# Kernel optimization log

Hardware: AMD Instinct MI355X
Metric: run time of the kernel (lower is better)

Reference implementation:

```python
import jax, jax.numpy as jnp
import numpy as np

N = 50000      # nodes in batched graph
E = 1600000    # edges (avg degree ~32)
D = 64         # feature width (features_dim = h_dim = out_dim)
R = 4          # num_rels (bond types)
L = 4          # RGCN layers: i2h + 2 hidden + h2o
B = 256        # graphs in the batch
NEG_SLOPE = 0.2


def setup_inputs() -> dict:
    key = jax.random.key(0)
    ks = jax.random.split(key, 12)
    h = jax.random.normal(ks[0], (N, D), jnp.float32)
    src = jax.random.randint(ks[1], (E,), 0, N, jnp.int32)
    dst = jax.random.randint(ks[2], (E,), 0, N, jnp.int32)
    etypes = jax.random.randint(ks[3], (E,), 0, R, jnp.int32)
    gids = jnp.sort(jax.random.randint(ks[4], (N,), 0, B, jnp.int32))
    Wrel = jax.random.normal(ks[5], (L, R, D, D), jnp.float32) * 0.05
    Wloop = jax.random.normal(ks[6], (L, D, D), jnp.float32) * 0.05
    brel = jnp.zeros((L, D), jnp.float32)
    Wg = jax.random.normal(ks[7], (D, D), jnp.float32) * 0.05
    al = jax.random.normal(ks[8], (D,), jnp.float32) * 0.05
    ar = jax.random.normal(ks[9], (D,), jnp.float32) * 0.05
    Wd = jax.random.normal(ks[10], (D, 1), jnp.float32) * 0.05
    bd = jnp.zeros((1,), jnp.float32)
    return dict(h=h, Wrel=Wrel, Wloop=Wloop, brel=brel, Wg=Wg, al=al, ar=ar,
                Wd=Wd, bd=bd, src=src, dst=dst, etypes=etypes, gids=gids)


def reference(h, Wrel, Wloop, brel, Wg, al, ar, Wd, bd, src, dst, etypes, gids):
    n = h.shape[0]
    # --- stacked RelGraphConv layers (basis regularizer with num_bases=num_rels
    # -> per-relation weight), self-loop + bias + ReLU, sum aggregation ---
    for l in range(Wrel.shape[0]):
        hr = jnp.einsum('nd,rdo->nro', h, Wrel[l])          # [N, R, D]
        msg = hr[src, etypes]                                # [E, D] gather
        agg = jax.ops.segment_sum(msg, dst, num_segments=n)  # [N, D] scatter-add
        h = jax.nn.relu(agg + h @ Wloop[l] + brel[l])
    # --- GATConv, 1 head ---
    z = h @ Wg                                               # [N, D]
    el = z @ al                                              # [N] a_l . z
    er = z @ ar                                              # [N] a_r . z
    e = jax.nn.leaky_relu(el[src] + er[dst], NEG_SLOPE)      # [E]
    m = jax.ops.segment_max(e, dst, num_segments=n)          # edge-softmax (stable)
    ex = jnp.exp(e - m[dst])
    den = jax.ops.segment_sum(ex, dst, num_segments=n)
    alpha = ex / jnp.maximum(den[dst], 1e-9)                 # [E]
    hg = jax.ops.segment_sum(alpha[:, None] * z[src], dst, num_segments=n)  # [N, D]
    # --- SumPooling over each graph, view [N,1,D] -> pooled [B,1,D] ---
    pooled = jax.ops.segment_sum(hg, gids, num_segments=B)[:, None, :]
    # --- dense head ---
    return pooled @ Wd + bd                                  # [B, 1, 1]
```

## Files before the change

### kernel.cpp

```cpp
#include <hip/hip_runtime.h>

#define DD 64
#define EPB 1024
#define NREP 8

typedef float f32x4 __attribute__((ext_vector_type(4)));
typedef float f32x8 __attribute__((ext_vector_type(8)));
typedef __bf16 bf16x8 __attribute__((ext_vector_type(8)));

__device__ __forceinline__ unsigned enc_f32(float x) {
  unsigned u = __float_as_uint(x);
  return (u & 0x80000000u) ? ~u : (u | 0x80000000u);
}
__device__ __forceinline__ float dec_f32(unsigned k) {
  return (k & 0x80000000u) ? __uint_as_float(k ^ 0x80000000u)
                           : __uint_as_float(~k);
}
__device__ __forceinline__ unsigned f2bf(float x) {
  unsigned u = __float_as_uint(x);
  return (u + 0x7fffu + ((u >> 16) & 1u)) >> 16;
}
__device__ __forceinline__ void unpack8(const uint4 raw, float* v) {
  v[0] = __uint_as_float(raw.x << 16);
  v[1] = __uint_as_float(raw.x & 0xffff0000u);
  v[2] = __uint_as_float(raw.y << 16);
  v[3] = __uint_as_float(raw.y & 0xffff0000u);
  v[4] = __uint_as_float(raw.z << 16);
  v[5] = __uint_as_float(raw.z & 0xffff0000u);
  v[6] = __uint_as_float(raw.w << 16);
  v[7] = __uint_as_float(raw.w & 0xffff0000u);
}
__device__ __forceinline__ f32x8 unpack8v(const uint4 r) {
  f32x8 v;
  v[0] = __uint_as_float(r.x << 16);
  v[1] = __uint_as_float(r.x & 0xffff0000u);
  v[2] = __uint_as_float(r.y << 16);
  v[3] = __uint_as_float(r.y & 0xffff0000u);
  v[4] = __uint_as_float(r.z << 16);
  v[5] = __uint_as_float(r.z & 0xffff0000u);
  v[6] = __uint_as_float(r.w << 16);
  v[7] = __uint_as_float(r.w & 0xffff0000u);
  return v;
}
__device__ __forceinline__ bf16x8 as_bf16x8(uint4 u) {
  union {
    uint4 u;
    bf16x8 b;
  } cv;
  cv.u = u;
  return cv.b;
}

__global__ __launch_bounds__(256) void f2_coarse(
    const int* __restrict__ src, const int* __restrict__ dst,
    const int* __restrict__ et, int* __restrict__ gcur,
    unsigned* __restrict__ staging, int E, int nfb,
    const float* __restrict__ h0, ushort* __restrict__ hbA, int n4) {
  __shared__ int lcnt[256];
  __shared__ int sc[256];
  __shared__ int lbase[256];
  __shared__ int gb[256];
  __shared__ unsigned rec[EPB];
  __shared__ unsigned char rbk[EPB];

  const int t = threadIdx.x;

  if (blockIdx.x >= nfb) {
    const int i = (blockIdx.x - nfb) * 256 + t;
    if (i < n4) {
      float4 v = ((const float4*)h0)[i];
      uint2 o;
      o.x = f2bf(v.x) | (f2bf(v.y) << 16);
      o.y = f2bf(v.z) | (f2bf(v.w) << 16);
      ((uint2*)hbA)[i] = o;
    }
    return;
  }

  const int base = blockIdx.x * EPB;
  const int rep = blockIdx.x & (NREP - 1);
  const int bc = min(EPB, E - base);

  lcnt[t] = 0;
  __syncthreads();

  int d_[EPB / 256], se_[EPB / 256], rk_[EPB / 256];
#pragma unroll
  for (int k = 0; k < EPB / 256; ++k) {
    const int e = base + k * 256 + t;
    if (e < E) {
      const int d = dst[e];
      d_[k] = d;
      se_[k] = (src[e] << 2) | et[e];
      rk_[k] = atomicAdd(&lcnt[d >> 8], 1);
    } else {
      d_[k] = -1;
    }
  }
  __syncthreads();

  const int lv = lcnt[t];
  sc[t] = lv;
  __syncthreads();
#pragma unroll
  for (int off = 1; off < 256; off <<= 1) {
    const int add = (t >= off) ? sc[t - off] : 0;
    __syncthreads();
    sc[t] += add;
    __syncthreads();
  }
  lbase[t] = sc[t] - lv;
  gb[t] = lv ? atomicAdd(&gcur[rep * 256 + t], lv) : 0;
  __syncthreads();

#pragma unroll
  for (int k = 0; k < EPB / 256; ++k) {
    if (d_[k] >= 0) {
      const int cb = d_[k] >> 8;
      const int pos = lbase[cb] + rk_[k];
      rec[pos] = ((unsigned)(d_[k] & 255) << 24) | (unsigned)se_[k];
      rbk[pos] = (unsigned char)cb;
    }
  }
  __syncthreads();

  for (int idx = t; idx < bc; idx += 256) {
    const int cb = rbk[idx];
    staging[gb[cb] + (idx - lbase[cb])] = rec[idx];
  }
}

__global__ __launch_bounds__(256) void cscan2(const int* __restrict__ gcur,
                                              int* __restrict__ cbase,
                                              int* __restrict__ rowptr, int N,
                                              int E, int CAP, int CAP8) {
  __shared__ int s[256];
  const int t = threadIdx.x;
  int c = 0;
#pragma unroll
  for (int r = 0; r < NREP; ++r)
    c += gcur[r * 256 + t] - (t * CAP + r * CAP8);
  s[t] = c;
  __syncthreads();
#pragma unroll
  for (int off = 1; off < 256; off <<= 1) {
    const int add = (t >= off) ? s[t - off] : 0;
    __syncthreads();
    s[t] += add;
    __syncthreads();
  }
  cbase[t] = s[t] - c;
  if (t == 0) rowptr[N] = E;
}

__global__ __launch_bounds__(256) void f3_fine4(
    const unsigned* __restrict__ staging, const int* __restrict__ gcur,
    const int* __restrict__ cbase, int* __restrict__ rowptr,
    int* __restrict__ srcet, int N, int CAP, int CAP8) {
  __shared__ int hist[256];
  __shared__ int sc[256];
  __shared__ int lcur[256];
  __shared__ int before;
  const int cb = blockIdx.x >> 2;
  const int sub = blockIdx.x & 3;
  const int t = threadIdx.x;
  const int dlo = sub << 6;

  hist[t] = 0;
  if (t == 0) before = 0;
  __syncthreads();

  int myb = 0;
#pragma unroll 1
  for (int r = 0; r < NREP; ++r) {
    const int s0 = cb * CAP + r * CAP8;
    const int s1 = gcur[r * 256 + cb];
    for (int i = s0 + t; i < s1; i += 256) {
      const unsigned rc = staging[i];
      const int dl = (int)(rc >> 24);
      const int off = dl - dlo;
      if ((unsigned)off < 64u)
        atomicAdd(&hist[(off << 2) | (int)(rc & 3u)], 1);
      else if (dl < dlo)
        ++myb;
    }
  }
#pragma unroll
  for (int off = 32; off > 0; off >>= 1) myb += __shfl_down(myb, off);
  if ((t & 63) == 0 && myb) atomicAdd(&before, myb);
  __syncthreads();

  const int v = hist[t];
  sc[t] = v;
  __syncthreads();
#pragma unroll
  for (int off = 1; off < 256; off <<= 1) {
    const int add = (t >= off) ? sc[t - off] : 0;
    __syncthreads();
    sc[t] += add;
    __syncthreads();
  }
  const int base = cbase[cb] + before + sc[t] - v;
  lcur[t] = base;
  if ((t & 3) == 0) {
    const int dn = (cb << 8) + dlo + (t >> 2);
    if (dn < N) rowptr[dn] = base;
  }
  __syncthreads();

#pragma unroll 1
  for (int r = 0; r < NREP; ++r) {
    const int s0 = cb * CAP + r * CAP8;
    const int s1 = gcur[r * 256 + cb];
    for (int i = s0 + t; i < s1; i += 256) {
      const unsigned rc = staging[i];
      const int dl = (int)(rc >> 24);
      const int off = dl - dlo;
      if ((unsigned)off < 64u) {
        const int pos = atomicAdd(&lcur[(off << 2) | (int)(rc & 3u)], 1);
        srcet[pos] = (int)(rc & 0xFFFFFFu);
      }
    }
  }
}

#define ACCUM8(se, v)                                                        \
  {                                                                          \
    const int r_ = (se) & 3;                                                 \
    if (r_ == 0) aA += (v);                                                  \
    else if (r_ == 1) aB += (v);                                             \
    else if (r_ == 2) aC += (v);                                             \
    else aD += (v);                                                          \
  }

#define RED8(a)                                                              \
  {                                                                          \
    a[0] += __shfl_xor(a[0], off); a[1] += __shfl_xor(a[1], off);            \
    a[2] += __shfl_xor(a[2], off); a[3] += __shfl_xor(a[3], off);            \
    a[4] += __shfl_xor(a[4], off); a[5] += __shfl_xor(a[5], off);            \
    a[6] += __shfl_xor(a[6], off); a[7] += __shfl_xor(a[7], off);            \
  }

__global__ __launch_bounds__(256) void gather_rel(
    const ushort* __restrict__ hb, const int* __restrict__ rowptr,
    const int* __restrict__ srcet, ushort* __restrict__ aggr_bf, int N) {
  const int n = blockIdx.x * 4 + (threadIdx.x >> 6);
  const int lane = threadIdx.x & 63;
  const int g = lane >> 3;
  const int t = lane & 7;
  if (n >= N) return;
  const int beg = rowptr[n], end = rowptr[n + 1];

  f32x8 aA = {0.f, 0.f, 0.f, 0.f, 0.f, 0.f, 0.f, 0.f};
  f32x8 aB = aA, aC = aA, aD = aA;

  int j = beg + g;
  for (; j + 24 < end; j += 32) {
    const int se0 = srcet[j];
    const int se1 = srcet[j + 8];
    const int se2 = srcet[j + 16];
    const int se3 = srcet[j + 24];
    const uint4 r0 = *(const uint4*)(hb + ((size_t)(se0 >> 2) << 6) + (t << 3));
    const uint4 r1 = *(const uint4*)(hb + ((size_t)(se1 >> 2) << 6) + (t << 3));
    const uint4 r2 = *(const uint4*)(hb + ((size_t)(se2 >> 2) << 6) + (t << 3));
    const uint4 r3 = *(const uint4*)(hb + ((size_t)(se3 >> 2) << 6) + (t << 3));
    const f32x8 v0 = unpack8v(r0);
    const f32x8 v1 = unpack8v(r1);
    const f32x8 v2 = unpack8v(r2);
    const f32x8 v3 = unpack8v(r3);
    ACCUM8(se0, v0);
    ACCUM8(se1, v1);
    ACCUM8(se2, v2);
    ACCUM8(se3, v3);
  }
  for (; j < end; j += 8) {
    const int se0 = srcet[j];
    const uint4 r0 = *(const uint4*)(hb + ((size_t)(se0 >> 2) << 6) + (t << 3));
    const f32x8 v0 = unpack8v(r0);
    ACCUM8(se0, v0);
  }

#pragma unroll
  for (int off = 8; off <= 32; off <<= 1) {
    RED8(aA);
    RED8(aB);
    RED8(aC);
    RED8(aD);
  }

  if (g < 4) {
    const f32x8 res = (g == 0) ? aA : (g == 1) ? aB : (g == 2) ? aC : aD;
    uint4 p;
    p.x = f2bf(res[0]) | (f2bf(res[1]) << 16);
    p.y = f2bf(res[2]) | (f2bf(res[3]) << 16);
    p.z = f2bf(res[4]) | (f2bf(res[5]) << 16);
    p.w = f2bf(res[6]) | (f2bf(res[7]) << 16);
    *(uint4*)(aggr_bf + ((size_t)n << 8) + (g << 6) + (t << 3)) = p;
  }
}

__global__ __launch_bounds__(256) void pack_w(
    const float* __restrict__ Wrel, const float* __restrict__ Wloop,
    const float* __restrict__ Wg, const float* __restrict__ al,
    const float* __restrict__ ar, const float* __restrict__ Wd,
    ushort* __restrict__ wpk, float* __restrict__ vav, int L,
    float* __restrict__ out, const float* __restrict__ bd, int out_n,
    unsigned* __restrict__ genc, int* __restrict__ gcur, int CAP, int CAP8) {
  const int l = blockIdx.x;
  if (l < L) {
    for (int f = threadIdx.x; f < 2560; f += 256) {
      const int lane = f & 63;
      const int kc = f >> 6;
      const int kt = kc >> 2;
      const int c = kc & 3;
      const int o = c * 16 + (lane & 15);
      const int kl0 = (lane >> 4) * 8;
      const float* wsrc =
          (kt < 8)
              ? Wrel + ((((size_t)l * 4 + (kt >> 1)) * 64 + (kt & 1) * 32 + kl0) * 64)
              : Wloop + (((size_t)l * 64 + (kt - 8) * 32 + kl0) * 64);
      unsigned o8[8];
#pragma unroll
      for (int j = 0; j < 8; ++j) o8[j] = f2bf(wsrc[(size_t)j * 64 + o]);
      uint4 p;
      p.x = o8[0] | (o8[1] << 16);
      p.y = o8[2] | (o8[3] << 16);
      p.z = o8[4] | (o8[5] << 16);
      p.w = o8[6] | (o8[7] << 16);
      *(uint4*)(wpk + (size_t)l * 20480 + (size_t)f * 8) = p;
    }
  } else if (l == L) {
    const int tt = threadIdx.x;
    if (tt < 192) {
      const int which = tt >> 6;
      const int d = tt & 63;
      const float* v = (which == 0) ? al : (which == 1) ? ar : Wd;
      float s = 0.f;
#pragma unroll
      for (int o = 0; o < 64; ++o) s = fmaf(Wg[d * 64 + o], v[o], s);
      vav[tt] = s;
    }
  } else {
    const int tt = threadIdx.x;
    for (int i = tt; i < out_n; i += 256) out[i] = bd[0];
    for (int i = tt; i < 256 * NREP; i += 256) {
      const int r = i >> 8;
      const int b = i & 255;
      gcur[i] = b * CAP + r * CAP8;
    }
    if (tt == 0) *genc = enc_f32(-1e30f);
  }
}

__global__ __launch_bounds__(256) void rgcn_dense_mfma(
    const ushort* __restrict__ aggr_bf, const ushort* __restrict__ hb_in,
    const ushort* __restrict__ wpk, const float* __restrict__ bias,
    ushort* __restrict__ hb_out, int N) {
  __shared__ __align__(16) char smraw[40960];
  const int tid = threadIdx.x;

  {
    const uint4* gsrc = (const uint4*)wpk;
    uint4* ldst = (uint4*)smraw;
#pragma unroll
    for (int i = 0; i < 10; ++i) ldst[i * 256 + tid] = gsrc[i * 256 + tid];
  }

  const int w = tid >> 6;
  const int lane = tid & 63;
  const int t = lane & 15;
  const int g = lane >> 4;
  const int n = blockIdx.x * 64 + w * 16 + t;
  const bool valid = n < N;

  f32x4 acc[4];
#pragma unroll
  for (int c = 0; c < 4; ++c) {
    const float b = bias[c * 16 + t];
    f32x4 z = {b, b, b, b};
    acc[c] = z;
  }

  __syncthreads();
  const bf16x8* bfr = (const bf16x8*)smraw;

#pragma unroll
  for (int kt = 0; kt < 10; ++kt) {
    uint4 raw = make_uint4(0u, 0u, 0u, 0u);
    if (valid) {
      const ushort* ap =
          (kt < 8) ? aggr_bf + (((size_t)n) << 8) + (kt << 5) + (g << 3)
                   : hb_in + (((size_t)n) << 6) + ((kt - 8) << 5) + (g << 3);
      raw = *(const uint4*)ap;
    }
    const bf16x8 a = as_bf16x8(raw);
#pragma unroll
    for (int c = 0; c < 4; ++c) {
      acc[c] = __builtin_amdgcn_mfma_f32_16x16x32_bf16(
          a, bfr[(kt * 4 + c) * 64 + lane], acc[c], 0, 0, 0);
    }
  }

  __syncthreads();
  float* tile = (float*)smraw;
  {
    const int r0 = w * 16 + g * 4;
#pragma unroll
    for (int c = 0; c < 4; ++c) {
      const int col = c * 16 + t;
#pragma unroll
      for (int r = 0; r < 4; ++r)
        tile[(r0 + r) * 65 + col] = fmaxf(acc[c][r], 0.f);
    }
  }
  __syncthreads();
  const int n0 = blockIdx.x * 64;
#pragma unroll
  for (int q = 0; q < 2; ++q) {
    const int f = q * 256 + tid;
    const int row = f >> 3;
    const int c8 = (f & 7) << 3;
    const int nn = n0 + row;
    if (nn < N) {
      const float* s = tile + row * 65 + c8;
      uint4 p;
      p.x = f2bf(s[0]) | (f2bf(s[1]) << 16);
      p.y = f2bf(s[2]) | (f2bf(s[3]) << 16);
      p.z = f2bf(s[4]) | (f2bf(s[5]) << 16);
      p.w = f2bf(s[6]) | (f2bf(s[7]) << 16);
      *(uint4*)(hb_out + (((size_t)nn) << 6) + c8) = p;
    }
  }
}

__global__ __launch_bounds__(256) void gat_proj(
    const ushort* __restrict__ hb, const float* __restrict__ vav,
    float2* __restrict__ ely, float* __restrict__ er,
    unsigned* __restrict__ genc, int N) {
  __shared__ float sv[192];
  const int tid = threadIdx.x;
  if (tid < 192) sv[tid] = vav[tid];
  __syncthreads();
  const int n = blockIdx.x * 256 + tid;
  float pl = 0.f, pr = 0.f, py = 0.f;
  if (n < N) {
    const ushort* row = hb + ((size_t)n << 6);
#pragma unroll
    for (int q = 0; q < 8; ++q) {
      const uint4 raw = *(const uint4*)(row + (q << 3));
      float v[8];
      unpack8(raw, v);
#pragma unroll
      for (int j = 0; j < 8; ++j) {
        pl = fmaf(v[j], sv[q * 8 + j], pl);
        pr = fmaf(v[j], sv[64 + q * 8 + j], pr);
        py = fmaf(v[j], sv[128 + q * 8 + j], py);
      }
    }
    ely[n] = make_float2(pl, py);
    er[n] = pr;
  }
  float mx = (n < N) ? pl : -1e30f;
#pragma unroll
  for (int off = 32; off > 0; off >>= 1) mx = fmaxf(mx, __shfl_xor(mx, off));
  if ((tid & 63) == 0) atomicMax(genc, enc_f32(mx));
}

#define GSC_NPG 2
#define GSC_NPB (16 * GSC_NPG)
__global__ __launch_bounds__(256) void gat_scalar(
    const float2* __restrict__ ely, const float* __restrict__ er,
    const int* __restrict__ rowptr, const int* __restrict__ srcet,
    const unsigned* __restrict__ genc, const int* __restrict__ gids,
    float* __restrict__ out, int N, int B) {
  __shared__ float acc[256];
  for (int i = threadIdx.x; i < B; i += 256) acc[i] = 0.f;
  __syncthreads();
  const int grp = threadIdx.x >> 4;
  const int ln = threadIdx.x & 15;
  const float gmax = dec_f32(*genc);
  const int base = blockIdx.x * GSC_NPB + grp * GSC_NPG;

#pragma unroll
  for (int i = 0; i < GSC_NPG; ++i) {
    const int n = base + i;
    if (n < N) {
      const int beg = rowptr[n], end = rowptr[n + 1];
      const float ern = er[n];
      float mb = gmax + ern;
      mb = (mb > 0.f) ? mb : 0.2f * mb;
      float num = 0.f, den = 0.f;
      for (int j = beg + ln; j < end; j += 16) {
        const float2 e2 = ely[srcet[j] >> 2];
        float x = e2.x + ern;
        x = (x > 0.f) ? x : 0.2f * x;
        const float w = __expf(x - mb);
        num = fmaf(w, e2.y, num);
        den += w;
      }
#pragma unroll
      for (int off = 1; off < 16; off <<= 1) {
        num += __shfl_xor(num, off);
        den += __shfl_xor(den, off);
      }
      if (ln == 0) atomicAdd(&acc[gids[n]], num / fmaxf(den, 1e-9f));
    }
  }
  __syncthreads();
  for (int i = threadIdx.x; i < B; i += 256) {
    const float v = acc[i];
    if (v != 0.f) unsafeAtomicAdd(out + i, v);
  }
}

extern "C" void kernel_launch(void* const* d_in, const int* in_sizes, int n_in,
                              void* d_out, int out_size, void* d_ws,
                              size_t ws_size, hipStream_t stream) {
  const float* h0 = (const float*)d_in[0];
  const float* Wrel = (const float*)d_in[1];
  const float* Wloop = (const float*)d_in[2];
  const float* brel = (const float*)d_in[3];
  const float* Wg = (const float*)d_in[4];
  const float* al = (const float*)d_in[5];
  const float* ar = (const float*)d_in[6];
  const float* Wd = (const float*)d_in[7];
  const float* bd = (const float*)d_in[8];
  const int* src = (const int*)d_in[9];
  const int* dst = (const int*)d_in[10];
  const int* et = (const int*)d_in[11];
  const int* gids = (const int*)d_in[12];

  const int N = in_sizes[0] / DD;
  const int E = in_sizes[9];
  const int L = in_sizes[2] / (DD * DD);
  float* out = (float*)d_out;
  const int CAP8 = ((E / (256 * NREP)) * 2 + 63) & ~63;
  const int CAP = CAP8 * NREP;

  char* wsb = (char*)d_ws;
  ushort* hbA = (ushort*)wsb;
  ushort* hbB = hbA + (size_t)N * DD;
  ushort* aggr_bf = hbB + (size_t)N * DD;
  int* rowptr = (int*)(aggr_bf + (size_t)N * 256);
  int* srcet = rowptr + N + 1;
  float2* ely = (float2*)(srcet + E);
  float* er = (float*)(ely + N);
  int* gcur = (int*)(er + N);
  int* cbase = gcur + 256 * NREP;
  unsigned* genc = (unsigned*)(cbase + 256);
  unsigned* staging = (unsigned*)aggr_bf;
  float* vav = (float*)(genc + 1);
  ushort* wpk = (ushort*)(((size_t)(char*)ely + 15) & ~(size_t)15);

  dim3 b256(256);
  const int grid_dense = (N + 63) / 64;
  const int nfb = (E + EPB - 1) / EPB;
  const int ncb = (N + 255) >> 8;
  const int n4 = N * DD / 4;
  const int ncv = (n4 + 255) / 256;

  hipLaunchKernelGGL(pack_w, dim3(L + 2), b256, 0, stream, Wrel, Wloop, Wg, al,
                     ar, Wd, wpk, vav, L, out, bd, out_size, genc, gcur, CAP,
                     CAP8);

  hipLaunchKernelGGL(f2_coarse, dim3(nfb + ncv), b256, 0, stream, src, dst, et,
                     gcur, staging, E, nfb, h0, hbA, n4);
  hipLaunchKernelGGL(cscan2, dim3(1), b256, 0, stream, gcur, cbase, rowptr, N,
                     E, CAP, CAP8);
  hipLaunchKernelGGL(f3_fine4, dim3(ncb * 4), b256, 0, stream, staging, gcur,
                     cbase, rowptr, srcet, N, CAP, CAP8);

  ushort* cur = hbA;
  ushort* nxt = hbB;
  for (int l = 0; l < L; ++l) {
    hipLaunchKernelGGL(gather_rel, dim3((N + 3) / 4), b256, 0, stream, cur,
                       rowptr, srcet, aggr_bf, N);
    hipLaunchKernelGGL(rgcn_dense_mfma, dim3(grid_dense), b256, 0, stream,
                       aggr_bf, cur, wpk + (size_t)l * 20480,
                       brel + (size_t)l * DD, nxt, N);
    ushort* tmp = cur; cur = nxt; nxt = tmp;
  }

  hipLaunchKernelGGL(gat_proj, dim3((N + 255) / 256), b256, 0, stream, cur, vav,
                     ely, er, genc, N);
  const int grid_gs = (N + GSC_NPB - 1) / GSC_NPB;
  hipLaunchKernelGGL(gat_scalar, dim3(grid_gs), b256, 0, stream, ely, er,
                     rowptr, srcet, genc, gids, out, N, out_size);
}
```

Baseline: 417.7 us.

## Split relational gather into two feature-half passes with 4-byte lanes

The per-layer gather is split into two launches, each covering 32 of the 64 bf16 feature columns. Within a wave, 16 lanes each load 4 bytes per edge and 4 edge groups run in parallel, replacing 8 lanes doing 16-byte loads across 8 edge groups. Each pass touches only half of every source row, which may raise L2 hit rates, and the index loads become nontemporal. The cost is that the edge index list and rowptr are read twice, there are twice as many gather launches, and each load is narrower.

```diff
diff --git a/kernel.cpp b/kernel.cpp
--- a/kernel.cpp
+++ b/kernel.cpp
@@ -5,7 +5,6 @@
 #define NREP 8
 
 typedef float f32x4 __attribute__((ext_vector_type(4)));
-typedef float f32x8 __attribute__((ext_vector_type(8)));
 typedef __bf16 bf16x8 __attribute__((ext_vector_type(8)));
 
 __device__ __forceinline__ unsigned enc_f32(float x) {
@@ -29,18 +28,6 @@
   v[5] = __uint_as_float(raw.z & 0xffff0000u);
   v[6] = __uint_as_float(raw.w << 16);
   v[7] = __uint_as_float(raw.w & 0xffff0000u);
-}
-__device__ __forceinline__ f32x8 unpack8v(const uint4 r) {
-  f32x8 v;
-  v[0] = __uint_as_float(r.x << 16);
-  v[1] = __uint_as_float(r.x & 0xffff0000u);
-  v[2] = __uint_as_float(r.y << 16);
-  v[3] = __uint_as_float(r.y & 0xffff0000u);
-  v[4] = __uint_as_float(r.z << 16);
-  v[5] = __uint_as_float(r.z & 0xffff0000u);
-  v[6] = __uint_as_float(r.w << 16);
-  v[7] = __uint_as_float(r.w & 0xffff0000u);
-  return v;
 }
 __device__ __forceinline__ bf16x8 as_bf16x8(uint4 u) {
   union {
@@ -224,79 +211,90 @@
   }
 }
 
-#define ACCUM8(se, v)                                                        \
+#define ACC2(se, vx, vy)                                                     \
   {                                                                          \
     const int r_ = (se) & 3;                                                 \
-    if (r_ == 0) aA += (v);                                                  \
-    else if (r_ == 1) aB += (v);                                             \
-    else if (r_ == 2) aC += (v);                                             \
-    else aD += (v);                                                          \
-  }
-
-#define RED8(a)                                                              \
-  {                                                                          \
-    a[0] += __shfl_xor(a[0], off); a[1] += __shfl_xor(a[1], off);            \
-    a[2] += __shfl_xor(a[2], off); a[3] += __shfl_xor(a[3], off);            \
-    a[4] += __shfl_xor(a[4], off); a[5] += __shfl_xor(a[5], off);            \
-    a[6] += __shfl_xor(a[6], off); a[7] += __shfl_xor(a[7], off);            \
-  }
-
-__global__ __launch_bounds__(256) void gather_rel(
+    if (r_ == 0) { a0x += vx; a0y += vy; }                                   \
+    else if (r_ == 1) { a1x += vx; a1y += vy; }                              \
+    else if (r_ == 2) { a2x += vx; a2y += vy; }                              \
+    else { a3x += vx; a3y += vy; }                                           \
+  }
+
+__global__ __launch_bounds__(256) void gather_rel_half(
     const ushort* __restrict__ hb, const int* __restrict__ rowptr,
-    const int* __restrict__ srcet, ushort* __restrict__ aggr_bf, int N) {
+    const int* __restrict__ srcet, ushort* __restrict__ aggr_bf, int N,
+    int half) {
   const int n = blockIdx.x * 4 + (threadIdx.x >> 6);
   const int lane = threadIdx.x & 63;
-  const int g = lane >> 3;
-  const int t = lane & 7;
+  const int g = lane >> 4;
+  const int t = lane & 15;
   if (n >= N) return;
   const int beg = rowptr[n], end = rowptr[n + 1];
-
-  f32x8 aA = {0.f, 0.f, 0.f, 0.f, 0.f, 0.f, 0.f, 0.f};
-  f32x8 aB = aA, aC = aA, aD = aA;
+  const ushort* hbh = hb + (half << 5) + (t << 1);
+
+  float a0x = 0.f, a0y = 0.f, a1x = 0.f, a1y = 0.f;
+  float a2x = 0.f, a2y = 0.f, a3x = 0.f, a3y = 0.f;
 
   int j = beg + g;
-  for (; j + 24 < end; j += 32) {
-    const int se0 = srcet[j];
-    const int se1 = srcet[j + 8];
-    const int se2 = srcet[j + 16];
-    const int se3 = srcet[j + 24];
-    const uint4 r0 = *(const uint4*)(hb + ((size_t)(se0 >> 2) << 6) + (t << 3));
-    const uint4 r1 = *(const uint4*)(hb + ((size_t)(se1 >> 2) << 6) + (t << 3));
-    const uint4 r2 = *(const uint4*)(hb + ((size_t)(se2 >> 2) << 6) + (t << 3));
-    const uint4 r3 = *(const uint4*)(hb + ((size_t)(se3 >> 2) << 6) + (t << 3));
-    const f32x8 v0 = unpack8v(r0);
-    const f32x8 v1 = unpack8v(r1);
-    const f32x8 v2 = unpack8v(r2);
-    const f32x8 v3 = unpack8v(r3);
-    ACCUM8(se0, v0);
-    ACCUM8(se1, v1);
-    ACCUM8(se2, v2);
-    ACCUM8(se3, v3);
-  }
-  for (; j < end; j += 8) {
-    const int se0 = srcet[j];
-    const uint4 r0 = *(const uint4*)(hb + ((size_t)(se0 >> 2) << 6) + (t << 3));
-    const f32x8 v0 = unpack8v(r0);
-    ACCUM8(se0, v0);
-  }
-
-#pragma unroll
-  for (int off = 8; off <= 32; off <<= 1) {
-    RED8(aA);
-    RED8(aB);
-    RED8(aC);
-    RED8(aD);
-  }
-
-  if (g < 4) {
-    const f32x8 res = (g == 0) ? aA : (g == 1) ? aB : (g == 2) ? aC : aD;
-    uint4 p;
-    p.x = f2bf(res[0]) | (f2bf(res[1]) << 16);
-    p.y = f2bf(res[2]) | (f2bf(res[3]) << 16);
-    p.z = f2bf(res[4]) | (f2bf(res[5]) << 16);
-    p.w = f2bf(res[6]) | (f2bf(res[7]) << 16);
-    *(uint4*)(aggr_bf + ((size_t)n << 8) + (g << 6) + (t << 3)) = p;
-  }
+  for (; j + 28 < end; j += 32) {
+    const int se0 = __builtin_nontemporal_load(srcet + j);
+    const int se1 = __builtin_nontemporal_load(srcet + j + 4);
+    const int se2 = __builtin_nontemporal_load(srcet + j + 8);
+    const int se3 = __builtin_nontemporal_load(srcet + j + 12);
+    const int se4 = __builtin_nontemporal_load(srcet + j + 16);
+    const int se5 = __builtin_nontemporal_load(srcet + j + 20);
+    const int se6 = __builtin_nontemporal_load(srcet + j + 24);
+    const int se7 = __builtin_nontemporal_load(srcet + j + 28);
+    const unsigned r0 = *(const unsigned*)(hbh + ((size_t)(se0 >> 2) << 6));
+    const unsigned r1 = *(const unsigned*)(hbh + ((size_t)(se1 >> 2) << 6));
+    const unsigned r2 = *(const unsigned*)(hbh + ((size_t)(se2 >> 2) << 6));
+    const unsigned r3 = *(const unsigned*)(hbh + ((size_t)(se3 >> 2) << 6));
+    const unsigned r4 = *(const unsigned*)(hbh + ((size_t)(se4 >> 2) << 6));
+    const unsigned r5 = *(const unsigned*)(hbh + ((size_t)(se5 >> 2) << 6));
+    const unsigned r6 = *(const unsigned*)(hbh + ((size_t)(se6 >> 2) << 6));
+    const unsigned r7 = *(const unsigned*)(hbh + ((size_t)(se7 >> 2) << 6));
+    ACC2(se0, __uint_as_float(r0 << 16), __uint_as_float(r0 & 0xffff0000u));
+    ACC2(se1, __uint_as_float(r1 << 16), __uint_as_float(r1 & 0xffff0000u));
+    ACC2(se2, __uint_as_float(r2 << 16), __uint_as_float(r2 & 0xffff0000u));
+    ACC2(se3, __uint_as_float(r3 << 16), __uint_as_float(r3 & 0xffff0000u));
+    ACC2(se4, __uint_as_float(r4 << 16), __uint_as_float(r4 & 0xffff0000u));
+    ACC2(se5, __uint_as_float(r5 << 16), __uint_as_float(r5 & 0xffff0000u));
+    ACC2(se6, __uint_as_float(r6 << 16), __uint_as_float(r6 & 0xffff0000u));
+    ACC2(se7, __uint_as_float(r7 << 16), __uint_as_float(r7 & 0xffff0000u));
+  }
+  for (; j + 12 < end; j += 16) {
+    const int se0 = __builtin_nontemporal_load(srcet + j);
+    const int se1 = __builtin_nontemporal_load(srcet + j + 4);
+    const int se2 = __builtin_nontemporal_load(srcet + j + 8);
+    const int se3 = __builtin_nontemporal_load(srcet + j + 12);
+    const unsigned r0 = *(const unsigned*)(hbh + ((size_t)(se0 >> 2) << 6));
+    const unsigned r1 = *(const unsigned*)(hbh + ((size_t)(se1 >> 2) << 6));
+    const unsigned r2 = *(const unsigned*)(hbh + ((size_t)(se2 >> 2) << 6));
+    const unsigned r3 = *(const unsigned*)(hbh + ((size_t)(se3 >> 2) << 6));
+    ACC2(se0, __uint_as_float(r0 << 16), __uint_as_float(r0 & 0xffff0000u));
+    ACC2(se1, __uint_as_float(r1 << 16), __uint_as_float(r1 & 0xffff0000u));
+    ACC2(se2, __uint_as_float(r2 << 16), __uint_as_float(r2 & 0xffff0000u));
+    ACC2(se3, __uint_as_float(r3 << 16), __uint_as_float(r3 & 0xffff0000u));
+  }
+  for (; j < end; j += 4) {
+    const int se0 = __builtin_nontemporal_load(srcet + j);
+    const unsigned r0 = *(const unsigned*)(hbh + ((size_t)(se0 >> 2) << 6));
+    ACC2(se0, __uint_as_float(r0 << 16), __uint_as_float(r0 & 0xffff0000u));
+  }
+
+#pragma unroll
+  for (int off = 16; off <= 32; off <<= 1) {
+    a0x += __shfl_xor(a0x, off); a0y += __shfl_xor(a0y, off);
+    a1x += __shfl_xor(a1x, off); a1y += __shfl_xor(a1y, off);
+    a2x += __shfl_xor(a2x, off); a2y += __shfl_xor(a2y, off);
+    a3x += __shfl_xor(a3x, off); a3y += __shfl_xor(a3y, off);
+  }
+
+  const float rx = (g == 0) ? a0x : (g == 1) ? a1x : (g == 2) ? a2x : a3x;
+  const float ry = (g == 0) ? a0y : (g == 1) ? a1y : (g == 2) ? a2y : a3y;
+  const unsigned p = f2bf(rx) | (f2bf(ry) << 16);
+  *(unsigned*)(aggr_bf + ((size_t)n << 8) + (g << 6) + (half << 5) + (t << 1)) =
+      p;
 }
 
 __global__ __launch_bounds__(256) void pack_w(
@@ -572,9 +570,12 @@
 
   ushort* cur = hbA;
   ushort* nxt = hbB;
+  const int grid_g = (N + 3) / 4;
   for (int l = 0; l < L; ++l) {
-    hipLaunchKernelGGL(gather_rel, dim3((N + 3) / 4), b256, 0, stream, cur,
-                       rowptr, srcet, aggr_bf, N);
+    hipLaunchKernelGGL(gather_rel_half, dim3(grid_g), b256, 0, stream, cur,
+                       rowptr, srcet, aggr_bf, N, 0);
+    hipLaunchKernelGGL(gather_rel_half, dim3(grid_g), b256, 0, stream, cur,
+                       rowptr, srcet, aggr_bf, N, 1);
     hipLaunchKernelGGL(rgcn_dense_mfma, dim3(grid_dense), b256, 0, stream,
                        aggr_bf, cur, wpk + (size_t)l * 20480,
                        brel + (size_t)l * DD, nxt, N);
```

After: 512.3 us. +22.6%, slower.
